# Performance work log

Measured on AMD Instinct MI355X. Metric: run time of the kernel, lower is better.

## Reference

```python
import jax, jax.numpy as jnp
import numpy as np

B, T, D, H, C = 256, 128, 1, 2048, 10


def _xavier(key, shape):
    fan_out, fan_in = shape
    std = float(np.sqrt(2.0 / (fan_in + fan_out)))
    return jax.random.normal(key, shape, dtype=jnp.float32) * std


def setup_inputs() -> dict:
    key = jax.random.key(0)
    kx, kU, kW, kV = jax.random.split(key, 4)
    return {
        "x": jax.random.normal(kx, (B, T), dtype=jnp.float32),
        "U": _xavier(kU, (H, D)),
        "W": _xavier(kW, (H, H)),
        "V": _xavier(kV, (C, H)),
        "bh": jnp.zeros((H,), dtype=jnp.float32),
        "bp": jnp.zeros((C,), dtype=jnp.float32),
    }


def reference(x, U, W, V, bh, bp):
    # x: [B, T]; per-step input x[:, t:t+1] -> [B, 1] (input_dim == 1)
    xs = jnp.swapaxes(x, 0, 1)[:, :, None]  # [T, B, 1]

    def step(h, x_t):
        # h: [B, H]; x_t: [B, 1]
        h_new = jnp.tanh(x_t @ U.T + h @ W.T + bh)
        return h_new, None

    h0 = jnp.zeros((x.shape[0], H), dtype=x.dtype)
    h_last, _ = jax.lax.scan(step, h0, xs)
    output = h_last @ V.T + bp  # [B, C]
    return (h_last, output)
```

## Files before the change

kernel.cpp:

```cpp
#include <hip/hip_runtime.h>
#include <cmath>


#define B_ 256
#define T_ 128
#define H_ 2048
#define C_ 10

typedef _Float16 half_t;
typedef _Float16 half8 __attribute__((ext_vector_type(8)));
typedef _Float16 half4v __attribute__((ext_vector_type(4)));
typedef float floatx4 __attribute__((ext_vector_type(4)));
typedef unsigned long long u64;
typedef unsigned long long u64x2 __attribute__((ext_vector_type(2)));

#define FLAG_DWORDS (128 * 8 * 32 * 32)

__device__ __forceinline__ float fast_tanh(float v) {
    return 1.0f - 2.0f / (__expf(2.0f * v) + 1.0f);
}

__device__ __forceinline__ void publish_u64(u64* p, u64 v) {
    u64 old = __hip_atomic_exchange(p, v, __ATOMIC_RELAXED,
                                    __HIP_MEMORY_SCOPE_AGENT);
    asm volatile("" :: "v"(old));
}

__global__ void __launch_bounds__(512, 2) rnn_persist(
    const float* __restrict__ x,
    const float* __restrict__ U,
    const float* __restrict__ W,
    const float* __restrict__ bh,
    const float* __restrict__ V,
    const float* __restrict__ bp,
    half_t* __restrict__ hP0,
    half_t* __restrict__ hP1,
    float* __restrict__ hf32,
    float* __restrict__ outp,
    unsigned* __restrict__ flags)
{
    const int tid  = threadIdx.x;
    const int wave = tid >> 6, lane = tid & 63;
    const int quad = lane >> 4, lq = lane & 15;
    const int id   = blockIdx.x;
    const int g    = id & 7;
    const int C    = id >> 3;
    const int m0   = g * 32;
    const int n0   = C * 64;

    half8 Bw[8][4];
#pragma unroll
    for (int kk = 0; kk < 8; ++kk) {
#pragma unroll
        for (int nt = 0; nt < 4; ++nt) {
            const int gn = n0 + nt * 16 + lq;
            const int k0 = wave * 256 + kk * 32 + quad * 8;
            const float4 w0 = *(const float4*)&W[(size_t)gn * H_ + k0];
            const float4 w1 = *(const float4*)&W[(size_t)gn * H_ + k0 + 4];
            const float wv[8] = {w0.x, w0.y, w0.z, w0.w, w1.x, w1.y, w1.z, w1.w};
            half8 hw;
#pragma unroll
            for (int j = 0; j < 8; ++j) hw[j] = (half_t)wv[j];
            Bw[kk][nt] = hw;
        }
    }

    const int mtO = wave & 1, ntO = wave >> 1;
    const float uvO = U[n0 + ntO * 16 + lq];
    const float bvO = bh[n0 + ntO * 16 + lq];

    __shared__ floatx4 red[2][8][4][64];
    __shared__ float Sm[32][65];
    __shared__ float xs[T_][32];

    for (int i = tid; i < 32 * T_; i += 512) {
        const int r = i & 31, tt = i >> 5;
        xs[tt][r] = x[(size_t)(m0 + r) * T_ + tt];
    }
    __syncthreads();

    const int prow = (tid >> 8) * 16 + ((tid >> 1) & 15);
    const int pcol = ((tid >> 7) & 1) * 32 + ((tid >> 5) & 3) * 8 + (tid & 1) * 4;
    const size_t slab = (size_t)g * 16384;
    const size_t pdst = slab + (size_t)C * 512 + tid;
    const size_t cbase = slab + (size_t)wave * 2048 + (size_t)lane * 2;

    unsigned* myflag_base = flags + ((size_t)g * 32 + C) * 32;
    const unsigned* pollp = flags + ((size_t)g * 32 + wave * 4 + (lane & 3)) * 32;

    {
        const float xb = xs[0][prow];
        half4v hv;
#pragma unroll
        for (int j = 0; j < 4; ++j) {
            const int n = n0 + pcol + j;
            hv[j] = (half_t)fast_tanh(xb * U[n] + bh[n]);
        }
        publish_u64((u64*)hP1 + pdst, __builtin_bit_cast(u64, hv));
    }
    __syncthreads();
    if (tid == 0)
        __hip_atomic_fetch_add(myflag_base, 1u, __ATOMIC_RELAXED,
                               __HIP_MEMORY_SCOPE_AGENT);

    for (int t = 1; t < T_; ++t) {
        const half_t* hin = (t & 1) ? hP1 : hP0;
        half_t* hout      = (t & 1) ? hP0 : hP1;
        const u64* pw = (const u64*)hin + cbase;

        {
            const unsigned* fp = pollp + (size_t)(t - 1) * (8 * 32 * 32);
            while (true) {
                const unsigned v = __hip_atomic_load(fp, __ATOMIC_RELAXED,
                                                     __HIP_MEMORY_SCOPE_AGENT);
                if (__all(v >= 1u)) break;
                __builtin_amdgcn_s_sleep(1);
            }
            asm volatile("" ::: "memory");
        }

        floatx4 acc[2][4] = {};

        u64 rl[16], rh[16];
        auto issue = [&](int f) {
            const u64* q = pw + (size_t)((f >> 2) * 512 + ((f >> 1) & 1) * 256
                                         + (f & 1) * 128);
            rl[f] = __hip_atomic_load(q, __ATOMIC_RELAXED,
                                      __HIP_MEMORY_SCOPE_AGENT);
            rh[f] = __hip_atomic_load(q + 1, __ATOMIC_RELAXED,
                                      __HIP_MEMORY_SCOPE_AGENT);
        };
#pragma unroll
        for (int f = 0; f < 16; ++f) issue(f);
#pragma unroll
        for (int f = 0; f < 16; ++f) {
            const int cp = f >> 2, mt = (f >> 1) & 1, kc = f & 1;
            const int kk = cp * 2 + kc;
            u64x2 bits; bits.x = rl[f]; bits.y = rh[f];
            const half8 av = __builtin_bit_cast(half8, bits);
            acc[mt][0] = __builtin_amdgcn_mfma_f32_16x16x32_f16(av, Bw[kk][0], acc[mt][0], 0, 0, 0);
            acc[mt][1] = __builtin_amdgcn_mfma_f32_16x16x32_f16(av, Bw[kk][1], acc[mt][1], 0, 0, 0);
            acc[mt][2] = __builtin_amdgcn_mfma_f32_16x16x32_f16(av, Bw[kk][2], acc[mt][2], 0, 0, 0);
            acc[mt][3] = __builtin_amdgcn_mfma_f32_16x16x32_f16(av, Bw[kk][3], acc[mt][3], 0, 0, 0);
        }

#pragma unroll
        for (int mt = 0; mt < 2; ++mt)
#pragma unroll
            for (int nt = 0; nt < 4; ++nt)
                red[mt][wave][nt][lane] = acc[mt][nt];
        __syncthreads();

        {
            float xr[4];
#pragma unroll
            for (int r = 0; r < 4; ++r) xr[r] = xs[t][mtO * 16 + quad * 4 + r];
            floatx4 s = red[mtO][0][ntO][lane];
#pragma unroll
            for (int ww = 1; ww < 8; ++ww) s += red[mtO][ww][ntO][lane];
#pragma unroll
            for (int r = 0; r < 4; ++r) {
                const float pre = s[r] + xr[r] * uvO + bvO;
                Sm[mtO * 16 + quad * 4 + r][ntO * 16 + lq] = fast_tanh(pre);
            }
        }
        __syncthreads();

        if (t < T_ - 1) {
            float fv[4];
#pragma unroll
            for (int j = 0; j < 4; ++j) fv[j] = Sm[prow][pcol + j];
            half4v hv;
#pragma unroll
            for (int j = 0; j < 4; ++j) hv[j] = (half_t)fv[j];
            publish_u64((u64*)hout + pdst, __builtin_bit_cast(u64, hv));
            __syncthreads();
            if (tid == 0)
                __hip_atomic_fetch_add(
                    myflag_base + (size_t)t * (8 * 32 * 32), 1u,
                    __ATOMIC_RELAXED, __HIP_MEMORY_SCOPE_AGENT);
        } else {
            {
                float fv[4];
#pragma unroll
                for (int j = 0; j < 4; ++j) fv[j] = Sm[prow][pcol + j];
                float* fd = hf32 + (size_t)(m0 + prow) * H_ + n0 + pcol;
                *(float4*)fd = make_float4(fv[0], fv[1], fv[2], fv[3]);
            }
            if (tid < 32 * C_) {
                const int r = tid & 31, c = tid >> 5;
                float s = (C == 0) ? bp[c] : 0.0f;
                const float* vr = V + (size_t)c * H_ + n0;
#pragma unroll 8
                for (int n = 0; n < 64; ++n) s += Sm[r][n] * vr[n];
                atomicAdd(&outp[(size_t)(m0 + r) * C_ + c], s);
            }
        }
    }
}

extern "C" void kernel_launch(void* const* d_in, const int* in_sizes, int n_in,
                              void* d_out, int out_size, void* d_ws, size_t ws_size,
                              hipStream_t stream) {
    const float* x  = (const float*)d_in[0];
    const float* U  = (const float*)d_in[1];
    const float* W  = (const float*)d_in[2];
    const float* V  = (const float*)d_in[3];
    const float* bh = (const float*)d_in[4];
    const float* bp = (const float*)d_in[5];

    float* out_h = (float*)d_out;
    float* outp  = out_h + (size_t)B_ * H_;

    half_t* hP0 = (half_t*)d_ws;
    half_t* hP1 = hP0 + (size_t)B_ * H_;
    unsigned* flags = (unsigned*)((char*)d_ws + 2u * 1024 * 1024);

    hipMemsetAsync(flags, 0, FLAG_DWORDS * sizeof(unsigned), stream);
    hipMemsetAsync(outp, 0, (size_t)B_ * C_ * sizeof(float), stream);

    rnn_persist<<<dim3(256), dim3(512), 0, stream>>>(
        x, U, W, bh, V, bp, hP0, hP1, out_h, outp, flags);
}
```

Measured before the change: 666.3 us.

## Use per-wave monotonic flags and double-buffered reduction to drop block barriers

Replaces the per-block flag, raised after a __syncthreads, with per-wave counters that increase monotonically. Each wave publishes its own transposed h tile and signals after draining its own memory ops, which removes two block-wide barriers per timestep. The reduction buffer is double-buffered so the next step can write without waiting on the previous step's reads. Loads of the previous h are split into two batches of eight interleaved with the MFMAs, reducing register pressure. Pollers now spin on eight per-wave flags per producer block, which adds more polling traffic, and correctness depends on the wave-level drain ordering the stores before the flag update.

```diff
diff --git a/kernel.cpp b/kernel.cpp
--- a/kernel.cpp
+++ b/kernel.cpp
@@ -14,7 +14,7 @@
 typedef unsigned long long u64;
 typedef unsigned long long u64x2 __attribute__((ext_vector_type(2)));
 
-#define FLAG_DWORDS (128 * 8 * 32 * 32)
+#define FLAG_DWORDS (256 * 8 * 32)
 
 __device__ __forceinline__ float fast_tanh(float v) {
     return 1.0f - 2.0f / (__expf(2.0f * v) + 1.0f);
@@ -24,6 +24,12 @@
     u64 old = __hip_atomic_exchange(p, v, __ATOMIC_RELAXED,
                                     __HIP_MEMORY_SCOPE_AGENT);
     asm volatile("" :: "v"(old));
+}
+
+__device__ __forceinline__ void wave_drain() {
+    __builtin_amdgcn_sched_barrier(0);
+    __builtin_amdgcn_s_waitcnt(0);
+    __builtin_amdgcn_sched_barrier(0);
 }
 
 __global__ void __launch_bounds__(512, 2) rnn_persist(
@@ -69,8 +75,8 @@
     const float uvO = U[n0 + ntO * 16 + lq];
     const float bvO = bh[n0 + ntO * 16 + lq];
 
-    __shared__ floatx4 red[2][8][4][64];
-    __shared__ float Sm[32][65];
+    __shared__ floatx4 red[2][2][8][4][64];
+    __shared__ __align__(16) float Tr[8][16][20];
     __shared__ float xs[T_][32];
 
     for (int i = tid; i < 32 * T_; i += 512) {
@@ -85,8 +91,13 @@
     const size_t pdst = slab + (size_t)C * 512 + tid;
     const size_t cbase = slab + (size_t)wave * 2048 + (size_t)lane * 2;
 
-    unsigned* myflag_base = flags + ((size_t)g * 32 + C) * 32;
-    const unsigned* pollp = flags + ((size_t)g * 32 + wave * 4 + (lane & 3)) * 32;
+    const int sigma = mtO * 256 + (ntO >> 1) * 128
+                    + ((ntO & 1) * 2 + (quad >> 1)) * 32 + lq * 2 + (quad & 1);
+    const size_t pdst_o = slab + (size_t)C * 512 + sigma;
+
+    unsigned* myflag = flags + (((size_t)(g * 32 + C)) * 8 + wave) * 32;
+    const unsigned* pollp = flags
+        + (((size_t)(g * 32 + wave * 4 + ((lane >> 3) & 3))) * 8 + (lane & 7)) * 32;
 
     {
         const float xb = xs[0][prow];
@@ -98,9 +109,9 @@
         }
         publish_u64((u64*)hP1 + pdst, __builtin_bit_cast(u64, hv));
     }
-    __syncthreads();
-    if (tid == 0)
-        __hip_atomic_fetch_add(myflag_base, 1u, __ATOMIC_RELAXED,
+    wave_drain();
+    if (lane == 0)
+        __hip_atomic_fetch_add(myflag, 1u, __ATOMIC_RELAXED,
                                __HIP_MEMORY_SCOPE_AGENT);
 
     for (int t = 1; t < T_; ++t) {
@@ -109,11 +120,10 @@
         const u64* pw = (const u64*)hin + cbase;
 
         {
-            const unsigned* fp = pollp + (size_t)(t - 1) * (8 * 32 * 32);
             while (true) {
-                const unsigned v = __hip_atomic_load(fp, __ATOMIC_RELAXED,
+                const unsigned v = __hip_atomic_load(pollp, __ATOMIC_RELAXED,
                                                      __HIP_MEMORY_SCOPE_AGENT);
-                if (__all(v >= 1u)) break;
+                if (__all(v >= (unsigned)t)) break;
                 __builtin_amdgcn_s_sleep(1);
             }
             asm volatile("" ::: "memory");
@@ -121,23 +131,24 @@
 
         floatx4 acc[2][4] = {};
 
-        u64 rl[16], rh[16];
+        u64 rl[8], rh[8];
         auto issue = [&](int f) {
             const u64* q = pw + (size_t)((f >> 2) * 512 + ((f >> 1) & 1) * 256
                                          + (f & 1) * 128);
-            rl[f] = __hip_atomic_load(q, __ATOMIC_RELAXED,
-                                      __HIP_MEMORY_SCOPE_AGENT);
-            rh[f] = __hip_atomic_load(q + 1, __ATOMIC_RELAXED,
-                                      __HIP_MEMORY_SCOPE_AGENT);
+            rl[f & 7] = __hip_atomic_load(q, __ATOMIC_RELAXED,
+                                          __HIP_MEMORY_SCOPE_AGENT);
+            rh[f & 7] = __hip_atomic_load(q + 1, __ATOMIC_RELAXED,
+                                          __HIP_MEMORY_SCOPE_AGENT);
         };
 #pragma unroll
-        for (int f = 0; f < 16; ++f) issue(f);
+        for (int f = 0; f < 8; ++f) issue(f);
 #pragma unroll
         for (int f = 0; f < 16; ++f) {
             const int cp = f >> 2, mt = (f >> 1) & 1, kc = f & 1;
             const int kk = cp * 2 + kc;
-            u64x2 bits; bits.x = rl[f]; bits.y = rh[f];
+            u64x2 bits; bits.x = rl[f & 7]; bits.y = rh[f & 7];
             const half8 av = __builtin_bit_cast(half8, bits);
+            if (f + 8 < 16) issue(f + 8);
             acc[mt][0] = __builtin_amdgcn_mfma_f32_16x16x32_f16(av, Bw[kk][0], acc[mt][0], 0, 0, 0);
             acc[mt][1] = __builtin_amdgcn_mfma_f32_16x16x32_f16(av, Bw[kk][1], acc[mt][1], 0, 0, 0);
             acc[mt][2] = __builtin_amdgcn_mfma_f32_16x16x32_f16(av, Bw[kk][2], acc[mt][2], 0, 0, 0);
@@ -148,52 +159,46 @@
         for (int mt = 0; mt < 2; ++mt)
 #pragma unroll
             for (int nt = 0; nt < 4; ++nt)
-                red[mt][wave][nt][lane] = acc[mt][nt];
+                red[t & 1][mt][wave][nt][lane] = acc[mt][nt];
         __syncthreads();
 
         {
             float xr[4];
 #pragma unroll
             for (int r = 0; r < 4; ++r) xr[r] = xs[t][mtO * 16 + quad * 4 + r];
-            floatx4 s = red[mtO][0][ntO][lane];
-#pragma unroll
-            for (int ww = 1; ww < 8; ++ww) s += red[mtO][ww][ntO][lane];
+            floatx4 s = red[t & 1][mtO][0][ntO][lane];
+#pragma unroll
+            for (int ww = 1; ww < 8; ++ww) s += red[t & 1][mtO][ww][ntO][lane];
 #pragma unroll
             for (int r = 0; r < 4; ++r) {
                 const float pre = s[r] + xr[r] * uvO + bvO;
-                Sm[mtO * 16 + quad * 4 + r][ntO * 16 + lq] = fast_tanh(pre);
+                Tr[wave][quad * 4 + r][lq] = fast_tanh(pre);
             }
-        }
-        __syncthreads();
-
-        if (t < T_ - 1) {
-            float fv[4];
-#pragma unroll
-            for (int j = 0; j < 4; ++j) fv[j] = Sm[prow][pcol + j];
-            half4v hv;
-#pragma unroll
-            for (int j = 0; j < 4; ++j) hv[j] = (half_t)fv[j];
-            publish_u64((u64*)hout + pdst, __builtin_bit_cast(u64, hv));
-            __syncthreads();
-            if (tid == 0)
-                __hip_atomic_fetch_add(
-                    myflag_base + (size_t)t * (8 * 32 * 32), 1u,
-                    __ATOMIC_RELAXED, __HIP_MEMORY_SCOPE_AGENT);
-        } else {
-            {
-                float fv[4];
-#pragma unroll
-                for (int j = 0; j < 4; ++j) fv[j] = Sm[prow][pcol + j];
-                float* fd = hf32 + (size_t)(m0 + prow) * H_ + n0 + pcol;
-                *(float4*)fd = make_float4(fv[0], fv[1], fv[2], fv[3]);
-            }
-            if (tid < 32 * C_) {
-                const int r = tid & 31, c = tid >> 5;
-                float s = (C == 0) ? bp[c] : 0.0f;
-                const float* vr = V + (size_t)c * H_ + n0;
+            const float4 fr = *(const float4*)&Tr[wave][lq][quad * 4];
+
+            if (t < T_ - 1) {
+                half4v hv;
+                hv[0] = (half_t)fr.x; hv[1] = (half_t)fr.y;
+                hv[2] = (half_t)fr.z; hv[3] = (half_t)fr.w;
+                publish_u64((u64*)hout + pdst_o, __builtin_bit_cast(u64, hv));
+                wave_drain();
+                if (lane == 0)
+                    __hip_atomic_fetch_add(myflag, 1u, __ATOMIC_RELAXED,
+                                           __HIP_MEMORY_SCOPE_AGENT);
+            } else {
+                float* fd = hf32 + (size_t)(m0 + mtO * 16 + lq) * H_
+                          + n0 + ntO * 16 + quad * 4;
+                *(float4*)fd = make_float4(fr.x, fr.y, fr.z, fr.w);
+                __syncthreads();
+                if (tid < 32 * C_) {
+                    const int r = tid & 31, c = tid >> 5;
+                    float sacc = (C == 0) ? bp[c] : 0.0f;
+                    const float* vr = V + (size_t)c * H_ + n0;
 #pragma unroll 8
-                for (int n = 0; n < 64; ++n) s += Sm[r][n] * vr[n];
-                atomicAdd(&outp[(size_t)(m0 + r) * C_ + c], s);
+                    for (int n = 0; n < 64; ++n)
+                        sacc += Tr[(n >> 4) * 2 + (r >> 4)][r & 15][n & 15] * vr[n];
+                    atomicAdd(&outp[(size_t)(m0 + r) * C_ + c], sacc);
+                }
             }
         }
     }
```

New measurement: 810.6 us. +21.6%, slower.
